# Kernel optimization log

Hardware: AMD Instinct MI355X
Metric: run time of the kernel (lower is better)

Reference implementation:

```python
import jax, jax.numpy as jnp
import numpy as np

TOP_K = 10        # top_k init arg
GAMMA = 0.7       # gamma init arg: weight on user's own prediction
TEMP = 0.5        # temperature for softmax over neighbor similarities
NEG_INF = -1e9    # used to exclude self from top-k (finite for bf16/fp16 safety)


def setup_inputs() -> dict:
    key = jax.random.key(0)
    k1, k2, k3 = jax.random.split(key, 3)
    N_USERS, N_ITEMS, BATCH = 8192, 4096, 2048
    # binary-ish user-item interaction matrix (sparse implicit feedback)
    full_user_vectors = (jax.random.uniform(k1, (N_USERS, N_ITEMS)) < 0.05).astype(jnp.float32)
    # diffusion-model denoised predictions for the batch
    predictions = jax.random.normal(k2, (BATCH, N_ITEMS), dtype=jnp.float32)
    batch_indices = jax.random.randint(k3, (BATCH,), 0, N_USERS)
    return {"predictions": predictions,
            "full_user_vectors": full_user_vectors,
            "batch_indices": batch_indices}


def reference(predictions, full_user_vectors, batch_indices):
    eps = 1e-8
    # cosine similarity matrix over all users: normalize rows, then GEMM
    norms = jnp.linalg.norm(full_user_vectors, axis=1, keepdims=True)
    normed = full_user_vectors / jnp.maximum(norms, eps)          # [N, I]
    sim = normed @ normed.T                                        # [N, N]
    n = sim.shape[0]
    diag = jnp.arange(n)
    sim = sim.at[diag, diag].set(NEG_INF)                          # exclude self
    # top-k similar users per user
    topk_sims, topk_idx = jax.lax.top_k(sim, TOP_K)                # [N, k]
    # gather for the batch
    b_sims = topk_sims[batch_indices]                              # [B, k]
    b_idx = topk_idx[batch_indices]                                # [B, k]
    weights = jax.nn.softmax(b_sims / TEMP, axis=-1)               # [B, k]
    neighbor_vecs = full_user_vectors[b_idx]                       # [B, k, I]
    agg = jnp.einsum('bk,bki->bi', weights, neighbor_vecs)         # [B, I]
    # gamma-weighted blend of own prediction and neighbor aggregate
    return GAMMA * predictions + (1.0 - GAMMA) * agg
```

## Files before the change

kernel.cpp:

```cpp
#include <hip/hip_runtime.h>
#include <hip/hip_bf16.h>

typedef int i32x4 __attribute__((ext_vector_type(4)));
typedef unsigned char uchar8 __attribute__((ext_vector_type(8)));
typedef unsigned char uchar4v __attribute__((ext_vector_type(4)));
typedef float float4v __attribute__((ext_vector_type(4)));
typedef unsigned long long u64;

#define N_USERS 8192
#define N_ITEMS 4096
#define BATCH   2048
#define TOPK    10

__device__ __forceinline__ void gload16(const unsigned char* src, char* dst) {
    __builtin_amdgcn_global_load_lds(
        (const __attribute__((address_space(1))) unsigned int*)src,
        (__attribute__((address_space(3))) unsigned int*)dst, 16, 0, 0);
}

__global__ __launch_bounds__(256)
void convert_rows(const float* __restrict__ A, unsigned char* __restrict__ Ai8,
                  float* __restrict__ invn) {
    __shared__ float wsum[4];
    const int row  = blockIdx.x;
    const int tid  = threadIdx.x;
    const int wave = tid >> 6;
    const int lane = tid & 63;
    const float* src = A + (size_t)row * N_ITEMS;
    unsigned char* dst = Ai8 + (size_t)row * N_ITEMS;
    float s = 0.f;
#pragma unroll
    for (int i = 0; i < 4; ++i) {
        const int col = tid * 4 + i * 1024;
        float4v v = *(const float4v*)(src + col);
        uchar4v o;
#pragma unroll
        for (int j = 0; j < 4; ++j) {
            o[j] = (unsigned char)(v[j] != 0.f);
            s += v[j];
        }
        *(uchar4v*)(dst + col) = o;
    }
#pragma unroll
    for (int o = 32; o > 0; o >>= 1) s += __shfl_down(s, o);
    if (lane == 0) wsum[wave] = s;
    __syncthreads();
    if (tid == 0) {
        float t = wsum[0] + wsum[1] + wsum[2] + wsum[3];
        invn[row] = (t > 0.f) ? (1.0f / sqrtf(t)) : 0.f;
    }
}

#define BAR_MID() do { __builtin_amdgcn_s_barrier(); \
    asm volatile("s_waitcnt lgkmcnt(0)" ::: "memory"); \
    __builtin_amdgcn_sched_barrier(0); \
    __builtin_amdgcn_s_setprio(1); } while (0)

#define BAR_END() do { __builtin_amdgcn_s_setprio(0); \
    __builtin_amdgcn_sched_barrier(0); \
    __builtin_amdgcn_s_barrier(); } while (0)

#define BAR_END_VM4() do { __builtin_amdgcn_s_setprio(0); \
    __builtin_amdgcn_sched_barrier(0); \
    asm volatile("s_waitcnt vmcnt(4)" ::: "memory"); \
    __builtin_amdgcn_sched_barrier(0); \
    __builtin_amdgcn_s_barrier(); } while (0)

#define BAR_END_VM0() do { __builtin_amdgcn_s_setprio(0); \
    __builtin_amdgcn_sched_barrier(0); \
    asm volatile("s_waitcnt vmcnt(0)" ::: "memory"); \
    __builtin_amdgcn_sched_barrier(0); \
    __builtin_amdgcn_s_barrier(); } while (0)

#define RD_A4(dst, bo, mofs) \
  _Pragma("unroll") for (int m_ = 0; m_ < 4; ++m_) { \
    dst[m_*2+0] = *(const i32x4*)(lds + (bo) + arowb + (m_+(mofs))*2048 + cb0); \
    dst[m_*2+1] = *(const i32x4*)(lds + (bo) + arowb + (m_+(mofs))*2048 + cb1); }

#define RD_B2(dst, bo, nofs) \
  _Pragma("unroll") for (int n_ = 0; n_ < 2; ++n_) { \
    dst[n_*2+0] = *(const i32x4*)(lds + (bo) + browb + (n_+(nofs))*2048 + cb0); \
    dst[n_*2+1] = *(const i32x4*)(lds + (bo) + browb + (n_+(nofs))*2048 + cb1); }

#define MMA4x2(afr, bfr, mofs, nofs) \
  _Pragma("unroll") for (int m_ = 0; m_ < 4; ++m_) \
  _Pragma("unroll") for (int n_ = 0; n_ < 2; ++n_) { \
    acc[m_+(mofs)][n_+(nofs)] = __builtin_amdgcn_mfma_i32_16x16x64_i8( \
        afr[m_*2+0], bfr[n_*2+0], acc[m_+(mofs)][n_+(nofs)], 0, 0, 0); \
    acc[m_+(mofs)][n_+(nofs)] = __builtin_amdgcn_mfma_i32_16x16x64_i8( \
        afr[m_*2+1], bfr[n_*2+1], acc[m_+(mofs)][n_+(nofs)], 0, 0, 0); }

#define WINDOW(bo, S0, S1, S2, S3, ENDW) do { \
    RD_A4(af,  bo, 0); RD_B2(bf01, bo, 0); S0; \
    BAR_MID(); MMA4x2(af,  bf01, 0, 0); BAR_END(); \
    RD_B2(bf23, bo, 2); S1; \
    BAR_MID(); MMA4x2(af,  bf23, 0, 2); BAR_END(); \
    RD_A4(af2, bo, 4); S2; \
    BAR_MID(); MMA4x2(af2, bf01, 4, 0); BAR_END(); \
    S3; \
    BAR_MID(); MMA4x2(af2, bf23, 4, 2); ENDW; \
} while (0)

__global__ __launch_bounds__(512, 2)
void sim_gemm8(const unsigned char* __restrict__ A,
               const int* __restrict__ bidx,
               const float* __restrict__ invn,
               float* __restrict__ sim) {
    __shared__ char lds[131072];

    const int tid  = threadIdx.x;
    const int w    = tid >> 6;
    const int lane = tid & 63;
    const int m0   = blockIdx.y * 256;
    const int n0   = blockIdx.x * 256;
    const int wr = w >> 2, wc = w & 3;

    const int fr = lane & 15, ks = lane >> 4;
    const int swz = (fr & 7) << 4;
    const int cb0 = (ks * 16) ^ swz;
    const int cb1 = (ks * 16 + 64) ^ swz;
    const int arowb = wr * 16384 + fr * 128;
    const int browb = 32768 + (wc >> 1) * 16384 + ((wc & 1) * 64 + fr) * 128;

    const int sr = lane >> 3;
    const int swzcolB = ((lane & 7) ^ sr) * 16;
    const unsigned char* pA[4];
    const unsigned char* pB[4];
#pragma unroll
    for (int g = 0; g < 4; ++g) {
        const int row = g * 64 + w * 8 + sr;
        pA[g] = A + (size_t)bidx[m0 + row] * N_ITEMS + swzcolB;
        pB[g] = A + (size_t)(n0 + row) * N_ITEMS + swzcolB;
    }

    i32x4 acc[8][4] = {};
    i32x4 af[8], af2[8], bf01[4], bf23[4];

#define STA(U, h) do { \
    char* d_ = lds + (((U) & 1) * 65536) + (h) * 16384 + w * 1024; \
    const int k0_ = (U) * 128; \
    gload16(pA[(h)*2+0] + k0_, d_); \
    gload16(pA[(h)*2+1] + k0_, d_ + 8192); } while (0)

#define STB(U, h) do { \
    char* d_ = lds + (((U) & 1) * 65536) + 32768 + (h) * 16384 + w * 1024; \
    const int k0_ = (U) * 128; \
    gload16(pB[(h)*2+0] + k0_, d_); \
    gload16(pB[(h)*2+1] + k0_, d_ + 8192); } while (0)

    STA(0, 0); STA(0, 1); STB(0, 0); STB(0, 1); STA(1, 0); STA(1, 1);
    asm volatile("s_waitcnt vmcnt(4)" ::: "memory");
    __builtin_amdgcn_s_barrier();

    for (int i = 0; i < 15; ++i) {
        const int t1 = 2 * i + 1, t2 = 2 * i + 2, t3 = 2 * i + 3;
        WINDOW(0,     STB(t1, 0), STB(t1, 1), STA(t2, 0), STA(t2, 1), BAR_END_VM4());
        WINDOW(65536, STB(t2, 0), STB(t2, 1), STA(t3, 0), STA(t3, 1), BAR_END_VM4());
    }
    WINDOW(0,     STB(31, 0), STB(31, 1), (void)0, (void)0, BAR_END_VM0());
    WINDOW(65536, (void)0, (void)0, (void)0, (void)0, BAR_END());

    const int crow_base = m0 + wr * 128 + ks * 4;
    const int ccol_base = n0 + wc * 64 + fr;
#pragma unroll
    for (int mf = 0; mf < 8; ++mf) {
#pragma unroll
        for (int j = 0; j < 4; ++j) {
            const int b  = crow_base + mf * 16 + j;
            const int ub = bidx[b];
            const float inb = invn[ub];
            float* rp = sim + (size_t)b * N_USERS;
#pragma unroll
            for (int nf = 0; nf < 4; ++nf) {
                const int nn = ccol_base + nf * 16;
                float v = (float)acc[mf][nf][j] * inb * invn[nn];
                if (nn == ub) v = -1e9f;
                rp[nn] = v;
            }
        }
    }
#undef STA
#undef STB
}

__device__ __forceinline__ u64 packkey(float f, int idx) {
    unsigned u = __float_as_uint(f);
    u = ((int)u < 0) ? ~u : (u | 0x80000000u);
    return ((u64)u << 32) | (unsigned)(~idx);
}

__global__ __launch_bounds__(256)
void select10(const float* __restrict__ sim, u64* __restrict__ keys) {
    const int wave = threadIdx.x >> 6;
    const int lane = threadIdx.x & 63;
    const int r    = blockIdx.x * 4 + wave;
    const float* sr = sim + (size_t)r * N_USERS;

    u64 cmax[32];
#pragma unroll
    for (int k = 0; k < 32; ++k) {
        const int slot = k * 64 + lane;
        float4v f = *(const float4v*)(sr + slot * 4);
        u64 a = packkey(f[0], slot * 4 + 0);
        u64 b = packkey(f[1], slot * 4 + 1);
        u64 c = packkey(f[2], slot * 4 + 2);
        u64 d = packkey(f[3], slot * 4 + 3);
        u64 ab = a > b ? a : b, cd = c > d ? c : d;
        cmax[k] = ab > cd ? ab : cd;
    }
    u64 lmax = cmax[0];
#pragma unroll
    for (int k = 1; k < 32; ++k) lmax = cmax[k] > lmax ? cmax[k] : lmax;

    u64 myout = 0;
#pragma unroll 1
    for (int it = 0; it < TOPK; ++it) {
        u64 wkey = lmax;
#pragma unroll
        for (int o = 1; o < 64; o <<= 1) {
            u64 ok = __shfl_xor(wkey, o);
            if (ok > wkey) wkey = ok;
        }
        if (lane == it) myout = wkey;
        const int widx = (int)(~(unsigned)wkey);
        const int slot = widx >> 2;
        if (lane == (slot & 63)) {
            const int kc = slot >> 6;
            float4v f = *(const float4v*)(sr + slot * 4);
            u64 m = 0;
#pragma unroll
            for (int j = 0; j < 4; ++j) {
                u64 kj = packkey(f[j], slot * 4 + j);
                if (kj < wkey && kj > m) m = kj;
            }
#pragma unroll
            for (int k = 0; k < 32; ++k) if (k == kc) cmax[k] = m;
            lmax = cmax[0];
#pragma unroll
            for (int k = 1; k < 32; ++k) lmax = cmax[k] > lmax ? cmax[k] : lmax;
        }
    }
    if (lane < TOPK) keys[(size_t)r * TOPK + lane] = myout;
}

__global__ __launch_bounds__(256)
void blend(const u64* __restrict__ keys,
           const unsigned char* __restrict__ Ai8,
           const float* __restrict__ pred,
           float* __restrict__ out) {
    const int b   = blockIdx.x;
    const int tid = threadIdx.x;

    float w[TOPK]; int nid[TOPK];
    float mx = -1e30f;
#pragma unroll
    for (int k = 0; k < TOPK; ++k) {
        u64 kk = keys[(size_t)b * TOPK + k];
        unsigned hi = (unsigned)(kk >> 32);
        unsigned bits = (hi & 0x80000000u) ? (hi ^ 0x80000000u) : ~hi;
        w[k] = __uint_as_float(bits);
        nid[k] = (int)(~(unsigned)kk);
        mx = fmaxf(mx, w[k]);
    }
    float sumw = 0.f;
#pragma unroll
    for (int k = 0; k < TOPK; ++k) {
        w[k] = __expf((w[k] - mx) * 2.0f);
        sumw += w[k];
    }
    const float scl = 0.3f / sumw;
#pragma unroll
    for (int k = 0; k < TOPK; ++k) w[k] *= scl;

    const float* pr = pred + (size_t)b * N_ITEMS;
    float*       po = out  + (size_t)b * N_ITEMS;
#pragma unroll
    for (int h = 0; h < 2; ++h) {
        const int col = h * 2048 + tid * 8;
        float4v p0 = *(const float4v*)(pr + col);
        float4v p1 = *(const float4v*)(pr + col + 4);
        float agg[8];
#pragma unroll
        for (int j = 0; j < 8; ++j) agg[j] = 0.f;
#pragma unroll
        for (int k = 0; k < TOPK; ++k) {
            uchar8 nv = *(const uchar8*)(Ai8 + (size_t)nid[k] * N_ITEMS + col);
#pragma unroll
            for (int j = 0; j < 8; ++j) agg[j] += w[k] * (float)nv[j];
        }
        float4v o0, o1;
#pragma unroll
        for (int j = 0; j < 4; ++j) {
            o0[j] = 0.7f * p0[j] + agg[j];
            o1[j] = 0.7f * p1[j] + agg[j + 4];
        }
        *(float4v*)(po + col)     = o0;
        *(float4v*)(po + col + 4) = o1;
    }
}

extern "C" void kernel_launch(void* const* d_in, const int* in_sizes, int n_in,
                              void* d_out, int out_size, void* d_ws, size_t ws_size,
                              hipStream_t stream) {
    const float* pred = (const float*)d_in[0];
    const float* A    = (const float*)d_in[1];
    const int*   bidx = (const int*)d_in[2];
    float*       out  = (float*)d_out;

    unsigned char* Ai8  = (unsigned char*)d_ws;
    float*         invn = (float*)((char*)d_ws + (size_t)N_USERS * N_ITEMS);
    float*         sim  = (float*)((char*)d_ws + (size_t)N_USERS * N_ITEMS + 65536);
    u64*           keys = (u64*)((char*)d_ws + (size_t)N_USERS * N_ITEMS + 65536
                                 + (size_t)BATCH * N_USERS * sizeof(float));

    convert_rows<<<N_USERS, 256, 0, stream>>>(A, Ai8, invn);
    sim_gemm8<<<dim3(N_USERS / 256, BATCH / 256), 512, 0, stream>>>(Ai8, bidx, invn, sim);
    select10<<<BATCH / 4, 256, 0, stream>>>(sim, keys);
    blend<<<BATCH, 256, 0, stream>>>(keys, Ai8, pred, out);
}
```

Baseline: 140.5 us.

## Fuse top-k selection into blend kernel with block-wide selection per row

```diff
diff --git a/kernel.cpp b/kernel.cpp
--- a/kernel.cpp
+++ b/kernel.cpp
@@ -190,76 +190,80 @@
 }
 
 __global__ __launch_bounds__(256)
-void select10(const float* __restrict__ sim, u64* __restrict__ keys) {
-    const int wave = threadIdx.x >> 6;
-    const int lane = threadIdx.x & 63;
-    const int r    = blockIdx.x * 4 + wave;
-    const float* sr = sim + (size_t)r * N_USERS;
-
-    u64 cmax[32];
-#pragma unroll
-    for (int k = 0; k < 32; ++k) {
-        const int slot = k * 64 + lane;
-        float4v f = *(const float4v*)(sr + slot * 4);
+void select_blend(const float* __restrict__ sim,
+                  const unsigned char* __restrict__ Ai8,
+                  const float* __restrict__ pred,
+                  float* __restrict__ out) {
+    __shared__ u64 bvs[256];
+
+    const int b    = blockIdx.x;
+    const int tid  = threadIdx.x;
+    const int lane = tid & 63;
+    const float* srow = sim + (size_t)b * N_USERS;
+
+    u64 cmax[8];
+#pragma unroll
+    for (int k = 0; k < 8; ++k) {
+        const int slot = tid + k * 256;
+        float4v f = ((const float4v*)srow)[slot];
         u64 a = packkey(f[0], slot * 4 + 0);
-        u64 b = packkey(f[1], slot * 4 + 1);
+        u64 bb = packkey(f[1], slot * 4 + 1);
         u64 c = packkey(f[2], slot * 4 + 2);
         u64 d = packkey(f[3], slot * 4 + 3);
-        u64 ab = a > b ? a : b, cd = c > d ? c : d;
+        u64 ab = a > bb ? a : bb, cd = c > d ? c : d;
         cmax[k] = ab > cd ? ab : cd;
     }
     u64 lmax = cmax[0];
 #pragma unroll
-    for (int k = 1; k < 32; ++k) lmax = cmax[k] > lmax ? cmax[k] : lmax;
-
-    u64 myout = 0;
-#pragma unroll 1
+    for (int k = 1; k < 8; ++k) lmax = cmax[k] > lmax ? cmax[k] : lmax;
+    bvs[tid] = lmax;
+    __syncthreads();
+
+    u64 topkeys[TOPK];
+#pragma unroll
     for (int it = 0; it < TOPK; ++it) {
-        u64 wkey = lmax;
+        u64 fv = bvs[lane];
+#pragma unroll
+        for (int g = 1; g < 4; ++g) {
+            u64 v2 = bvs[lane + g * 64];
+            if (v2 > fv) fv = v2;
+        }
 #pragma unroll
         for (int o = 1; o < 64; o <<= 1) {
-            u64 ok = __shfl_xor(wkey, o);
-            if (ok > wkey) wkey = ok;
-        }
-        if (lane == it) myout = wkey;
-        const int widx = (int)(~(unsigned)wkey);
+            u64 ok = __shfl_xor(fv, o);
+            if (ok > fv) fv = ok;
+        }
+        topkeys[it] = fv;
+        __syncthreads();
+        const int widx = (int)(~(unsigned)fv);
         const int slot = widx >> 2;
-        if (lane == (slot & 63)) {
-            const int kc = slot >> 6;
-            float4v f = *(const float4v*)(sr + slot * 4);
+        if (tid == (slot & 255)) {
+            const int kc = slot >> 8;
+            float4v f = *(const float4v*)(srow + slot * 4);
             u64 m = 0;
 #pragma unroll
             for (int j = 0; j < 4; ++j) {
                 u64 kj = packkey(f[j], slot * 4 + j);
-                if (kj < wkey && kj > m) m = kj;
+                if (kj < fv && kj > m) m = kj;
             }
 #pragma unroll
-            for (int k = 0; k < 32; ++k) if (k == kc) cmax[k] = m;
-            lmax = cmax[0];
-#pragma unroll
-            for (int k = 1; k < 32; ++k) lmax = cmax[k] > lmax ? cmax[k] : lmax;
-        }
-    }
-    if (lane < TOPK) keys[(size_t)r * TOPK + lane] = myout;
-}
-
-__global__ __launch_bounds__(256)
-void blend(const u64* __restrict__ keys,
-           const unsigned char* __restrict__ Ai8,
-           const float* __restrict__ pred,
-           float* __restrict__ out) {
-    const int b   = blockIdx.x;
-    const int tid = threadIdx.x;
+            for (int k = 0; k < 8; ++k) if (k == kc) cmax[k] = m;
+            u64 nl = cmax[0];
+#pragma unroll
+            for (int k = 1; k < 8; ++k) nl = cmax[k] > nl ? cmax[k] : nl;
+            bvs[tid] = nl;
+        }
+        __syncthreads();
+    }
 
     float w[TOPK]; int nid[TOPK];
     float mx = -1e30f;
 #pragma unroll
     for (int k = 0; k < TOPK; ++k) {
-        u64 kk = keys[(size_t)b * TOPK + k];
-        unsigned hi = (unsigned)(kk >> 32);
+        unsigned hi = (unsigned)(topkeys[k] >> 32);
         unsigned bits = (hi & 0x80000000u) ? (hi ^ 0x80000000u) : ~hi;
         w[k] = __uint_as_float(bits);
-        nid[k] = (int)(~(unsigned)kk);
+        nid[k] = (int)(~(unsigned)topkeys[k]);
         mx = fmaxf(mx, w[k]);
     }
     float sumw = 0.f;
@@ -310,11 +314,8 @@
     unsigned char* Ai8  = (unsigned char*)d_ws;
     float*         invn = (float*)((char*)d_ws + (size_t)N_USERS * N_ITEMS);
     float*         sim  = (float*)((char*)d_ws + (size_t)N_USERS * N_ITEMS + 65536);
-    u64*           keys = (u64*)((char*)d_ws + (size_t)N_USERS * N_ITEMS + 65536
-                                 + (size_t)BATCH * N_USERS * sizeof(float));
 
     convert_rows<<<N_USERS, 256, 0, stream>>>(A, Ai8, invn);
     sim_gemm8<<<dim3(N_USERS / 256, BATCH / 256), 512, 0, stream>>>(Ai8, bidx, invn, sim);
-    select10<<<BATCH / 4, 256, 0, stream>>>(sim, keys);
-    blend<<<BATCH, 256, 0, stream>>>(keys, Ai8, pred, out);
-}
+    select_blend<<<BATCH, 256, 0, stream>>>(sim, Ai8, pred, out);
+}
```

Result: faster. 134.1 us (-4.5%).
